# Kernel optimization log

Hardware: AMD Instinct MI355X
Metric: run time of the kernel (lower is better)

Reference implementation:

```python
import jax, jax.numpy as jnp
import numpy as np

B, L, C, D, H = 32, 4096, 64, 512, 720
EPS = 1e-5

def _xavier(key, shape):
    fan_in, fan_out = shape
    lim = float(np.sqrt(6.0 / (fan_in + fan_out)))
    return jax.random.uniform(key, shape, minval=-lim, maxval=lim, dtype=jnp.float32)

def setup_inputs() -> dict:
    key = jax.random.key(0)
    ks = jax.random.split(key, 8)
    return {
        "x": jax.random.normal(ks[0], (B, L, C), dtype=jnp.float32),
        "alpha": jnp.full((C,), 0.5, dtype=jnp.float32),
        "rev_w": jnp.ones((C,), dtype=jnp.float32),
        "rev_b": jnp.zeros((C,), dtype=jnp.float32),
        "se_w": _xavier(ks[1], (C, D)), "se_b": jnp.zeros((D,), jnp.float32),
        "sp_w": _xavier(ks[2], (D, C)), "sp_b": jnp.zeros((C,), jnp.float32),
        "st_w": _xavier(ks[3], (L, H)), "st_b": jnp.zeros((H,), jnp.float32),
        "te_w": _xavier(ks[4], (C, D)), "te_b": jnp.zeros((D,), jnp.float32),
        "tp_w": _xavier(ks[5], (D, C)), "tp_b": jnp.zeros((C,), jnp.float32),
        "tt_w": _xavier(ks[6], (L, H)), "tt_b": jnp.zeros((H,), jnp.float32),
    }

def _path(z, ew, eb, pw, pb, tw, tb):
    # z: (B,L,C) -> embed C->D -> (identity backbone) -> proj D->C -> temporal L->H
    h = z @ ew + eb            # (B,L,D)
    h = h @ pw + pb            # (B,L,C)
    h = jnp.einsum('blc,lh->bhc', h, tw) + tb[None, :, None]  # (B,H,C)
    return h

def reference(x, alpha, rev_w, rev_b, se_w, se_b, sp_w, sp_b, st_w, st_b,
              te_w, te_b, tp_w, tp_b, tt_w, tt_b):
    # RevIN norm (stats detached, var unbiased=False)
    mean = jax.lax.stop_gradient(jnp.mean(x, axis=1, keepdims=True))          # (B,1,C)
    stdev = jax.lax.stop_gradient(jnp.sqrt(jnp.var(x, axis=1, keepdims=True) + EPS))
    xn = (x - mean) / stdev * rev_w + rev_b
    # EMA decomposition: trend[t] = a*trend[t-1] + (1-a)*x[t], trend[0]=x[0]
    a = jax.nn.sigmoid(alpha)  # (C,)
    def step(carry, xt):
        nxt = a * carry + (1.0 - a) * xt
        return nxt, nxt
    t0 = xn[:, 0]                                    # (B,C)
    _, tr = jax.lax.scan(step, t0, jnp.swapaxes(xn, 0, 1)[1:])  # (L-1,B,C)
    trend = jnp.swapaxes(jnp.concatenate([t0[None], tr], axis=0), 0, 1)  # (B,L,C)
    seasonal = xn - trend
    out = _path(seasonal, se_w, se_b, sp_w, sp_b, st_w, st_b) \
        + _path(trend,    te_w, te_b, tp_w, tp_b, tt_w, tt_b)   # (B,H,C)
    # RevIN denorm
    out = (out - rev_b) / (rev_w + EPS)
    out = out * stdev + mean
    return out
```

## Files before the change

### kernel.cpp

```cpp
#include <hip/hip_runtime.h>
#include <hip/hip_bf16.h>
#include <string.h>
#include <stdint.h>

typedef __hip_bfloat16 bf16_t;
typedef float f32x4 __attribute__((ext_vector_type(4)));
typedef short bf16x8 __attribute__((ext_vector_type(8)));

static constexpr int Bn = 32, Ln = 4096, Cn = 64, Hn = 720, HPn = 768;
static constexpr float EPSf = 1e-5f;

static constexpr size_t OSR_SLICE = (size_t)Bn * Hn * Cn;

__device__ __forceinline__ short f2bf(float f) {
  bf16_t h = __float2bfloat16(f);
  unsigned short u; memcpy(&u, &h, 2);
  return (short)u;
}

__device__ __forceinline__ float sigm(float v) { return 1.f / (1.f + expf(-v)); }

__global__ void __launch_bounds__(256) k_pre(
    const float* __restrict__ se_w, const float* __restrict__ sp_w,
    const float* __restrict__ se_b, const float* __restrict__ sp_b,
    const float* __restrict__ te_w, const float* __restrict__ tp_w,
    const float* __restrict__ te_b, const float* __restrict__ tp_b,
    const float* __restrict__ st_w, const float* __restrict__ tt_w,
    const float* __restrict__ x, const float* __restrict__ alpha,
    float* __restrict__ M, float* __restrict__ cvec, bf16_t* __restrict__ Wt,
    float* __restrict__ Spart,
    float* __restrict__ Psub, float* __restrict__ Pseg,
    float* __restrict__ Ssum, float* __restrict__ Ssq) {
  __shared__ __align__(16) char smem[35072];
  int bid = blockIdx.x, t = threadIdx.x;

  if (bid < 2) {
    float (*ews)[68] = (float(*)[68])smem;
    float (*pws)[68] = (float(*)[68])(smem + 17408);
    float* ebs = (float*)(smem + 34816);
    int p = bid;
    const float* ew = p ? te_w : se_w;
    const float* pw = p ? tp_w : sp_w;
    const float* eb = p ? te_b : se_b;
    const float* pb = p ? tp_b : sp_b;
    int r0 = (t >> 4) * 4, c0 = (t & 15) * 4;
    float acc[4][4];
#pragma unroll
    for (int i = 0; i < 4; ++i)
#pragma unroll
      for (int j = 0; j < 4; ++j) acc[i][j] = 0.f;
    float cv = 0.f;
    for (int dc = 0; dc < 8; ++dc) {
      int d0 = dc * 64;
#pragma unroll
      for (int q = 0; q < 4; ++q) {
        int fi = t * 4 + q;
        int r = fi >> 4, dd = (fi * 4) & 63;
        *reinterpret_cast<f32x4*>(&ews[r][dd]) = *reinterpret_cast<const f32x4*>(&ew[r * 512 + d0 + dd]);
        *reinterpret_cast<f32x4*>(&pws[r][dd]) = *reinterpret_cast<const f32x4*>(&pw[(d0 + r) * 64 + dd]);
      }
      if (t < 64) ebs[t] = eb[d0 + t];
      __syncthreads();
#pragma unroll 4
      for (int g = 0; g < 16; ++g) {
        int dd = g * 4;
        f32x4 av[4], bv[4];
#pragma unroll
        for (int i = 0; i < 4; ++i) av[i] = *reinterpret_cast<const f32x4*>(&ews[r0 + i][dd]);
#pragma unroll
        for (int d = 0; d < 4; ++d) bv[d] = *reinterpret_cast<const f32x4*>(&pws[dd + d][c0]);
#pragma unroll
        for (int d = 0; d < 4; ++d)
#pragma unroll
          for (int i = 0; i < 4; ++i)
#pragma unroll
            for (int j = 0; j < 4; ++j) acc[i][j] = fmaf(av[i][d], bv[d][j], acc[i][j]);
      }
      if (t < 64) {
#pragma unroll 8
        for (int dd = 0; dd < 64; ++dd) cv = fmaf(ebs[dd], pws[dd][t], cv);
      }
      __syncthreads();
    }
#pragma unroll
    for (int i = 0; i < 4; ++i)
#pragma unroll
      for (int j = 0; j < 4; ++j)
        M[p * 4096 + (r0 + i) * 64 + c0 + j] = acc[i][j];
    if (t < 64) cvec[p * 64 + t] = cv + pb[t];

  } else if (bid < 514) {
    float (*lp)[64] = (float(*)[64])smem;
    float (*ls)[64] = (float(*)[64])(smem + 4096);
    float (*lq)[64] = (float(*)[64])(smem + 8192);
    int idx = bid - 2;
    int b = idx >> 4, sg = idx & 15;
    int ty = t >> 6, tx = t & 63;
    int s = sg * 4 + ty;
    int c4 = (tx & 15) * 4, sub = tx >> 4;
    float a[4], k1[4];
#pragma unroll
    for (int i = 0; i < 4; ++i) { a[i] = sigm(alpha[c4 + i]); k1[i] = 1.f - a[i]; }
    const float* xb = x + ((size_t)b * Ln + s * 64 + sub * 16) * Cn + c4;
    float pr[4] = {0.f, 0.f, 0.f, 0.f}, sm[4] = {0.f, 0.f, 0.f, 0.f}, sq[4] = {0.f, 0.f, 0.f, 0.f};
#pragma unroll
    for (int j = 0; j < 16; ++j) {
      f32x4 v = *reinterpret_cast<const f32x4*>(xb + (size_t)j * Cn);
#pragma unroll
      for (int i = 0; i < 4; ++i) {
        sm[i] += v[i];
        sq[i] = fmaf(v[i], v[i], sq[i]);
        pr[i] = fmaf(a[i], pr[i], k1[i] * v[i]);
      }
    }
    *reinterpret_cast<f32x4*>(&Psub[(((size_t)b * 64 + s) * 4 + sub) * 64 + c4]) =
        (f32x4){pr[0], pr[1], pr[2], pr[3]};
#pragma unroll
    for (int i = 0; i < 4; ++i) {
      lp[ty * 4 + sub][c4 + i] = pr[i];
      ls[ty * 4 + sub][c4 + i] = sm[i];
      lq[ty * 4 + sub][c4 + i] = sq[i];
    }
    __syncthreads();
    int c = tx;
    float av = sigm(alpha[c]);
    float a16 = av * av; a16 *= a16; a16 *= a16; a16 *= a16;
    float P = ((lp[ty * 4 + 0][c] * a16 + lp[ty * 4 + 1][c]) * a16 + lp[ty * 4 + 2][c]) * a16 + lp[ty * 4 + 3][c];
    int oidx = (b * 64 + s) * 64 + c;
    Pseg[oidx] = P;
    Ssum[oidx] = ls[ty * 4 + 0][c] + ls[ty * 4 + 1][c] + ls[ty * 4 + 2][c] + ls[ty * 4 + 3][c];
    Ssq[oidx]  = lq[ty * 4 + 0][c] + lq[ty * 4 + 1][c] + lq[ty * 4 + 2][c] + lq[ty * 4 + 3][c];

  } else {
    float (*tile)[65] = (float(*)[65])smem;
    float (*colsum)[64] = (float(*)[64])(smem + 16640);
    int idx = bid - 514;
    int p = idx / 768, rem = idx % 768;
    int lc = rem & 63, hc = rem >> 6;
    const float* W = p ? tt_w : st_w;
    int l0 = lc * 64, h0 = hc * 64;
    int row = t >> 6, col = t & 63;
    int h = h0 + col;
    float partial = 0.f;
    for (int r = row; r < 64; r += 4) {
      float v = (h < Hn) ? W[(size_t)(l0 + r) * Hn + h] : 0.f;
      tile[r][col] = v;
      partial += v;
    }
    colsum[row][col] = partial;
    __syncthreads();
    if (row == 0)
      Spart[((size_t)p * 64 + lc) * 768 + h] = colsum[0][col] + colsum[1][col] + colsum[2][col] + colsum[3][col];
    short* AF = (short*)Wt + (size_t)p * HPn * Ln;
#pragma unroll
    for (int u = 0; u < 2; ++u) {
      int uid = u * 256 + t;
      int ln = uid & 63, ktl = (uid >> 6) & 1, htl = uid >> 7;
      int fr = ln & 15, hi = ln >> 4;
      int ll = ktl * 32 + hi * 8;
      int hh = htl * 16 + fr;
      bf16x8 v;
#pragma unroll
      for (int e = 0; e < 8; ++e) v[e] = f2bf(tile[ll + e][hh]);
      size_t ht = (size_t)(h0 >> 4) + htl, ktg = (size_t)(l0 >> 5) + ktl;
      *reinterpret_cast<bf16x8*>(&AF[((ht * 128 + ktg) << 9) + ((size_t)ln << 3)]) = v;
    }
  }
}

__global__ void __launch_bounds__(256) k_mid(
    const float* __restrict__ x, const float* __restrict__ alpha,
    const float* __restrict__ rev_w, const float* __restrict__ rev_b,
    const float* __restrict__ Pseg, const float* __restrict__ Ssum, const float* __restrict__ Ssq,
    const float* __restrict__ Spart,
    float* __restrict__ mean, float* __restrict__ rstd, float* __restrict__ stdv,
    float* __restrict__ CarryIn, float* __restrict__ S) {
  int bid = blockIdx.x, t = threadIdx.x;
  if (bid < 8) {
    int b = bid * 4 + (t >> 6), c = t & 63;
    float sm = 0.f, sq = 0.f;
#pragma unroll 8
    for (int s = 0; s < 64; ++s) {
      int idx = (b * 64 + s) * 64 + c;
      sm += Ssum[idx]; sq += Ssq[idx];
    }
    float mn = sm * (1.f / 4096.f);
    float var = sq * (1.f / 4096.f) - mn * mn;
    float sd = sqrtf(var + EPSf);
    float rs = 1.f / sd;
    mean[b * 64 + c] = mn; stdv[b * 64 + c] = sd; rstd[b * 64 + c] = rs;

    float w = rev_w[c], rb = rev_b[c];
    float g = rs * w, d = rb - mn * g;
    float a = sigm(alpha[c]);
    float a2 = a * a, a4 = a2 * a2, a8 = a4 * a4, a16 = a8 * a8, a32 = a16 * a16;
    float a64 = a32 * a32;
    float dk1s = d * (1.f - a64);
    float carry = fmaf(g, x[((size_t)b * Ln) * Cn + c], d);
    for (int so = 0; so < 8; ++so) {
      float pv[8];
#pragma unroll
      for (int i = 0; i < 8; ++i)
        pv[i] = Pseg[((size_t)(b * 64 + so * 8 + i)) * 64 + c];
#pragma unroll
      for (int i = 0; i < 8; ++i) {
        CarryIn[((size_t)(b * 64 + so * 8 + i)) * 64 + c] = carry;
        carry = fmaf(a64, carry, fmaf(g, pv[i], dk1s));
      }
    }
  } else {
    int idx = (bid - 8) * 256 + t;
    int p = idx / 768, h = idx % 768;
    float s = 0.f;
#pragma unroll 8
    for (int lc = 0; lc < 64; ++lc)
      s += Spart[((size_t)p * 64 + lc) * 768 + h];
    S[p * 768 + h] = s;
  }
}

__global__ void __launch_bounds__(256) k_scanC(const float* __restrict__ x, const float* __restrict__ alpha,
                                               const float* __restrict__ rev_w, const float* __restrict__ rev_b,
                                               const float* __restrict__ mean, const float* __restrict__ rstd,
                                               const float* __restrict__ CarryIn, const float* __restrict__ Psub,
                                               bf16_t* __restrict__ Zt) {
  int b = blockIdx.x, ty = threadIdx.y, s = blockIdx.y * 4 + ty, t = threadIdx.x;
  int c4 = (t & 15) * 4, sub = t >> 4;
  float g[4], d[4], a[4], k1[4], a16[4], dk[4], tr[4];
#pragma unroll
  for (int i = 0; i < 4; ++i) {
    int c = c4 + i;
    float rs = rstd[b * 64 + c];
    g[i] = rs * rev_w[c]; d[i] = rev_b[c] - mean[b * 64 + c] * g[i];
    a[i] = sigm(alpha[c]); k1[i] = 1.f - a[i];
    float v = a[i] * a[i]; v *= v; v *= v; v *= v;
    a16[i] = v;
    dk[i] = d[i] * (1.f - v);
  }
  f32x4 cs = *reinterpret_cast<const f32x4*>(&CarryIn[((size_t)b * 64 + s) * 64 + c4]);
#pragma unroll
  for (int i = 0; i < 4; ++i) tr[i] = cs[i];
  for (int k = 0; k < sub; ++k) {
    f32x4 p = *reinterpret_cast<const f32x4*>(&Psub[(((size_t)b * 64 + s) * 4 + k) * 64 + c4]);
#pragma unroll
    for (int i = 0; i < 4; ++i) tr[i] = fmaf(a16[i], tr[i], fmaf(g[i], p[i], dk[i]));
  }
  const float* xb = x + ((size_t)b * Ln + s * 64 + sub * 16) * Cn + c4;
  bf16x8 vs[4][2], vt[4][2];
#pragma unroll
  for (int j = 0; j < 16; ++j) {
    f32x4 v = *reinterpret_cast<const f32x4*>(xb + (size_t)j * Cn);
#pragma unroll
    for (int i = 0; i < 4; ++i) {
      float xn = fmaf(g[i], v[i], d[i]);
      tr[i] = fmaf(a[i], tr[i], k1[i] * xn);
      vs[i][j >> 3][j & 7] = f2bf(xn - tr[i]);
      vt[i][j >> 3][j & 7] = f2bf(tr[i]);
    }
  }
  __shared__ short stage[4][8][520];
  short* BF0 = (short*)Zt;
  const size_t PATH = (size_t)Bn * Cn * Ln;
  int cq = (t & 15) >> 2;
  int u = cq * 2 + (sub >> 1);
  int hb = (sub & 1) * 2;
#pragma unroll
  for (int i = 0; i < 4; ++i) {
    int frv = (c4 & 15) + i;
    *reinterpret_cast<bf16x8*>(&stage[ty][u][(hb * 16 + frv) * 8]) = vs[i][0];
    *reinterpret_cast<bf16x8*>(&stage[ty][u][((hb + 1) * 16 + frv) * 8]) = vs[i][1];
  }
#pragma unroll
  for (int uu = 0; uu < 8; ++uu) {
    size_t nt = (size_t)b * 4 + (uu >> 1), ktg = (size_t)s * 2 + (uu & 1);
    *reinterpret_cast<bf16x8*>(BF0 + ((nt * 128 + ktg) << 9) + ((size_t)t << 3)) =
        *reinterpret_cast<const bf16x8*>(&stage[ty][uu][t * 8]);
  }
#pragma unroll
  for (int i = 0; i < 4; ++i) {
    int frv = (c4 & 15) + i;
    *reinterpret_cast<bf16x8*>(&stage[ty][u][(hb * 16 + frv) * 8]) = vt[i][0];
    *reinterpret_cast<bf16x8*>(&stage[ty][u][((hb + 1) * 16 + frv) * 8]) = vt[i][1];
  }
#pragma unroll
  for (int uu = 0; uu < 8; ++uu) {
    size_t nt = (size_t)b * 4 + (uu >> 1), ktg = (size_t)s * 2 + (uu & 1);
    *reinterpret_cast<bf16x8*>(BF0 + PATH + ((nt * 128 + ktg) << 9) + ((size_t)t << 3)) =
        *reinterpret_cast<const bf16x8*>(&stage[ty][uu][t * 8]);
  }
}

template <int KS>
__global__ void __launch_bounds__(256, 3) k_gemm(const bf16_t* __restrict__ Wt, const bf16_t* __restrict__ Zt,
                                                 float* __restrict__ Osr) {
  int per = gridDim.x >> 3;
  int swz = (blockIdx.x & 7) * per + (blockIdx.x >> 3);
  int z = swz / 96, rem = swz % 96;
  int by = rem >> 4, bx = rem & 15;
  int p = z / KS, kq = z % KS;
  const short* AF = (const short*)Wt + (size_t)p * HPn * Ln;
  const short* BF = (const short*)Zt + (size_t)p * (Bn * Cn) * Ln;
  int h0 = by * 128, n0 = bx * 128;
  int kbase = kq * (Ln / KS);
  const int NT = (Ln / KS) / 32;
  int tid = threadIdx.x, wid = tid >> 6, lane = tid & 63;
  int wr = wid >> 1, wc = wid & 1;
  int fr = lane & 15, hi = lane >> 4;
  const short* ab = AF + ((((size_t)(h0 >> 4) + wr * 4) * 128 + (kbase >> 5)) << 9) + ((size_t)lane << 3);
  const short* bb = BF + ((((size_t)(n0 >> 4) + wc * 4) * 128 + (kbase >> 5)) << 9) + ((size_t)lane << 3);

  f32x4 acc[4][4];
#pragma unroll
  for (int i = 0; i < 4; ++i)
#pragma unroll
    for (int j = 0; j < 4; ++j) acc[i][j] = (f32x4){0.f, 0.f, 0.f, 0.f};

  auto LOAD = [&](bf16x8 (&a)[4], bf16x8 (&b)[4], int kt) {
#pragma unroll
    for (int i = 0; i < 4; ++i)
      a[i] = *reinterpret_cast<const bf16x8*>(ab + (((size_t)i * 128 + kt) << 9));
#pragma unroll
    for (int j = 0; j < 4; ++j)
      b[j] = *reinterpret_cast<const bf16x8*>(bb + (((size_t)j * 128 + kt) << 9));
  };
  auto COMPUTE = [&](const bf16x8 (&a)[4], const bf16x8 (&b)[4]) {
    __builtin_amdgcn_s_setprio(1);
#pragma unroll
    for (int i = 0; i < 4; ++i)
#pragma unroll
      for (int j = 0; j < 4; ++j)
        acc[i][j] = __builtin_amdgcn_mfma_f32_16x16x32_bf16(a[i], b[j], acc[i][j], 0, 0, 0);
    __builtin_amdgcn_s_setprio(0);
  };

  bf16x8 aA[4], bA[4], aB[4], bB[4];
  LOAD(aA, bA, 0);
  for (int t = 0; t < NT; t += 2) {
    if (t + 1 < NT) LOAD(aB, bB, t + 1);
    __builtin_amdgcn_s_barrier();
    COMPUTE(aA, bA);
    if (t + 2 < NT) LOAD(aA, bA, t + 2);
    __builtin_amdgcn_s_barrier();
    if (t + 1 < NT) COMPUTE(aB, bB);
  }

#pragma unroll
  for (int i = 0; i < 4; ++i) {
#pragma unroll
    for (int j = 0; j < 4; ++j) {
#pragma unroll
      for (int r = 0; r < 4; ++r) {
        int m = wr * 64 + i * 16 + hi * 4 + r;
        int h = h0 + m;
        if (h < Hn) {
          int n = n0 + wc * 64 + j * 16 + fr;
          int bidx = n >> 6, c = n & 63;
          Osr[(((size_t)z * Bn + bidx) * Hn + h) * Cn + c] = acc[i][j][r];
        }
      }
    }
  }
}

template <int KS>
__global__ void __launch_bounds__(256) k_epi(const float* __restrict__ Osr, const float* __restrict__ M,
                                             const float* __restrict__ cvec, const float* __restrict__ S,
                                             const float* __restrict__ st_b, const float* __restrict__ tt_b,
                                             const float* __restrict__ rev_w, const float* __restrict__ rev_b,
                                             const float* __restrict__ mean, const float* __restrict__ stdv,
                                             float* __restrict__ out) {
  __shared__ float Msh[2][64][64];
  __shared__ float rowS[32][64];
  __shared__ float rowT[32][64];
  int t = threadIdx.x;
  for (int i = t; i < 2048; i += 256)
    reinterpret_cast<f32x4*>(Msh)[i] = reinterpret_cast<const f32x4*>(M)[i];
  int c = t & 63, grp = t >> 6;
  float w = rev_w[c], rb = rev_b[c];
  float cs = cvec[c], ct = cvec[64 + c];
  int base = blockIdx.x * 32;
#pragma unroll
  for (int k = 0; k < 8; ++k) {
    int rl = grp * 8 + k;
    int r = base + rl;
    int b = r / 720, h = r % 720;
    float vs = 0.f, vt = 0.f;
#pragma unroll
    for (int kq = 0; kq < KS; ++kq) {
      vs += Osr[(((size_t)kq * Bn + b) * Hn + h) * Cn + c];
      vt += Osr[(((size_t)(KS + kq) * Bn + b) * Hn + h) * Cn + c];
    }
    rowS[rl][c] = vs;
    rowT[rl][c] = vt;
  }
  __syncthreads();
  float acc[8];
  int hh[8], bb[8];
#pragma unroll
  for (int k = 0; k < 8; ++k) {
    int r = base + grp * 8 + k;
    bb[k] = r / 720; hh[k] = r % 720;
    acc[k] = cs * S[hh[k]] + ct * S[768 + hh[k]] + st_b[hh[k]] + tt_b[hh[k]];
  }
  int r0 = grp * 8;
  for (int cq = 0; cq < 16; ++cq) {
    f32x4 rs[8], rt[8];
#pragma unroll
    for (int k = 0; k < 8; ++k) rs[k] = *reinterpret_cast<const f32x4*>(&rowS[r0 + k][cq * 4]);
#pragma unroll
    for (int k = 0; k < 8; ++k) rt[k] = *reinterpret_cast<const f32x4*>(&rowT[r0 + k][cq * 4]);
#pragma unroll
    for (int i = 0; i < 4; ++i) {
      float m0 = Msh[0][cq * 4 + i][c], m1 = Msh[1][cq * 4 + i][c];
#pragma unroll
      for (int k = 0; k < 8; ++k)
        acc[k] = fmaf(rs[k][i], m0, fmaf(rt[k][i], m1, acc[k]));
    }
  }
  float winv = 1.f / (w + EPSf);
#pragma unroll
  for (int k = 0; k < 8; ++k) {
    float o = (acc[k] - rb) * winv * stdv[bb[k] * Cn + c] + mean[bb[k] * Cn + c];
    out[(size_t)(base + r0 + k) * 64 + c] = o;
  }
}

extern "C" void kernel_launch(void* const* d_in, const int* in_sizes, int n_in,
                              void* d_out, int out_size, void* d_ws, size_t ws_size,
                              hipStream_t stream) {
  const float* x     = (const float*)d_in[0];
  const float* alpha = (const float*)d_in[1];
  const float* rev_w = (const float*)d_in[2];
  const float* rev_b = (const float*)d_in[3];
  const float* se_w  = (const float*)d_in[4];
  const float* se_b  = (const float*)d_in[5];
  const float* sp_w  = (const float*)d_in[6];
  const float* sp_b  = (const float*)d_in[7];
  const float* st_w  = (const float*)d_in[8];
  const float* st_b  = (const float*)d_in[9];
  const float* te_w  = (const float*)d_in[10];
  const float* te_b  = (const float*)d_in[11];
  const float* tp_w  = (const float*)d_in[12];
  const float* tp_b  = (const float*)d_in[13];
  const float* tt_w  = (const float*)d_in[14];
  const float* tt_b  = (const float*)d_in[15];
  float* out = (float*)d_out;

  const size_t SZ_WT  = (size_t)2 * HPn * Ln * 2;
  const size_t SZ_ZT  = (size_t)2 * Bn * Cn * Ln * 2;
  const size_t SZ_SEG = (size_t)Bn * 64 * 64 * 4;
  const size_t SZ_M   = 2 * 64 * 64 * 4;
  const size_t SZ_CV  = 2 * 64 * 4;
  const size_t SZ_S   = 2 * 768 * 4;
  const size_t SZ_SP  = (size_t)2 * 64 * 768 * 4;
  const size_t TAIL   = SZ_M + SZ_CV + SZ_S + SZ_SP + 3 * (size_t)Bn * Cn * 4;

  const size_t NEED4 = SZ_WT + SZ_ZT + 8 * OSR_SLICE * 4 + TAIL;
  const int KS = (ws_size >= NEED4) ? 4 : 1;
  const size_t SZ_OSR = (size_t)(2 * KS) * OSR_SLICE * 4;

  char* ws = (char*)d_ws;
  bf16_t* Wt   = (bf16_t*)(ws);
  bf16_t* Zt   = (bf16_t*)(ws + SZ_WT);
  float*  Osr  = (float*)(ws + SZ_WT + SZ_ZT);
  float*  Psub  = Osr;
  float*  Pseg  = (float*)((char*)Psub + 4 * SZ_SEG);
  float*  Ssum  = (float*)((char*)Pseg + SZ_SEG);
  float*  Ssq   = (float*)((char*)Ssum + SZ_SEG);
  float*  Carry = (float*)((char*)Ssq + SZ_SEG);
  char* tail = ws + SZ_WT + SZ_ZT + SZ_OSR;
  float* Mbuf = (float*)tail;                 tail += SZ_M;
  float* cvec = (float*)tail;                 tail += SZ_CV;
  float* S    = (float*)tail;                 tail += SZ_S;
  float* Spart = (float*)tail;                tail += SZ_SP;
  float* mean = (float*)tail;                 tail += (size_t)Bn * Cn * 4;
  float* rstd = (float*)tail;                 tail += (size_t)Bn * Cn * 4;
  float* stdv = (float*)tail;

  k_pre<<<2050, 256, 0, stream>>>(se_w, sp_w, se_b, sp_b, te_w, tp_w, te_b, tp_b,
                                  st_w, tt_w, x, alpha, Mbuf, cvec, Wt, Spart,
                                  Psub, Pseg, Ssum, Ssq);
  k_mid<<<14, 256, 0, stream>>>(x, alpha, rev_w, rev_b, Pseg, Ssum, Ssq, Spart,
                                mean, rstd, stdv, Carry, S);
  k_scanC<<<dim3(32, 16), dim3(64, 4), 0, stream>>>(x, alpha, rev_w, rev_b, mean, rstd, Carry, Psub, Zt);
  if (KS == 4) {
    k_gemm<4><<<768, 256, 0, stream>>>(Wt, Zt, Osr);
    k_epi<4><<<720, 256, 0, stream>>>(Osr, Mbuf, cvec, S, st_b, tt_b, rev_w, rev_b, mean, stdv, out);
  } else {
    k_gemm<1><<<192, 256, 0, stream>>>(Wt, Zt, Osr);
    k_epi<1><<<720, 256, 0, stream>>>(Osr, Mbuf, cvec, S, st_b, tt_b, rev_w, rev_b, mean, stdv, out);
  }
}
```

Measured before the change: 108.0 us.

## Move weight-product and column-sum blocks off the critical path into GEMM launch

New measurement: 109.5 us. No clear change (+1.4%).

```diff
diff --git a/kernel.cpp b/kernel.cpp
--- a/kernel.cpp
+++ b/kernel.cpp
@@ -20,80 +20,67 @@
 
 __device__ __forceinline__ float sigm(float v) { return 1.f / (1.f + expf(-v)); }
 
-__global__ void __launch_bounds__(256) k_pre(
-    const float* __restrict__ se_w, const float* __restrict__ sp_w,
-    const float* __restrict__ se_b, const float* __restrict__ sp_b,
-    const float* __restrict__ te_w, const float* __restrict__ tp_w,
-    const float* __restrict__ te_b, const float* __restrict__ tp_b,
+__global__ void __launch_bounds__(256) k_preA(
     const float* __restrict__ st_w, const float* __restrict__ tt_w,
     const float* __restrict__ x, const float* __restrict__ alpha,
-    float* __restrict__ M, float* __restrict__ cvec, bf16_t* __restrict__ Wt,
-    float* __restrict__ Spart,
+    bf16_t* __restrict__ Wt, float* __restrict__ Spart,
     float* __restrict__ Psub, float* __restrict__ Pseg,
     float* __restrict__ Ssum, float* __restrict__ Ssq) {
-  __shared__ __align__(16) char smem[35072];
+  __shared__ __align__(16) char smem[20736];
   int bid = blockIdx.x, t = threadIdx.x;
 
-  if (bid < 2) {
-    float (*ews)[68] = (float(*)[68])smem;
-    float (*pws)[68] = (float(*)[68])(smem + 17408);
-    float* ebs = (float*)(smem + 34816);
-    int p = bid;
-    const float* ew = p ? te_w : se_w;
-    const float* pw = p ? tp_w : sp_w;
-    const float* eb = p ? te_b : se_b;
-    const float* pb = p ? tp_b : sp_b;
-    int r0 = (t >> 4) * 4, c0 = (t & 15) * 4;
-    float acc[4][4];
-#pragma unroll
-    for (int i = 0; i < 4; ++i)
-#pragma unroll
-      for (int j = 0; j < 4; ++j) acc[i][j] = 0.f;
-    float cv = 0.f;
-    for (int dc = 0; dc < 8; ++dc) {
-      int d0 = dc * 64;
-#pragma unroll
-      for (int q = 0; q < 4; ++q) {
-        int fi = t * 4 + q;
-        int r = fi >> 4, dd = (fi * 4) & 63;
-        *reinterpret_cast<f32x4*>(&ews[r][dd]) = *reinterpret_cast<const f32x4*>(&ew[r * 512 + d0 + dd]);
-        *reinterpret_cast<f32x4*>(&pws[r][dd]) = *reinterpret_cast<const f32x4*>(&pw[(d0 + r) * 64 + dd]);
+  if (bid < 1536) {
+    float (*tile)[65] = (float(*)[65])smem;
+    float (*cs16)[64] = (float(*)[64])(smem + 16640);
+    int p = bid / 768, rem = bid % 768;
+    int lc = rem & 63, hc = rem >> 6;
+    const float* W = p ? tt_w : st_w;
+    int l0 = lc * 64, h0 = hc * 64;
+    int g16 = t >> 4, c4l = (t & 15) * 4;
+    int h = h0 + c4l;
+    f32x4 ps = (f32x4){0.f, 0.f, 0.f, 0.f};
+#pragma unroll
+    for (int rr = 0; rr < 4; ++rr) {
+      int r = rr * 16 + g16;
+      const float* src = &W[(size_t)(l0 + r) * Hn + h];
+      f32x4 v;
+      if (h + 3 < Hn) {
+        v = *reinterpret_cast<const f32x4*>(src);
+      } else {
+#pragma unroll
+        for (int i = 0; i < 4; ++i) v[i] = (h + i < Hn) ? src[i] : 0.f;
       }
-      if (t < 64) ebs[t] = eb[d0 + t];
-      __syncthreads();
-#pragma unroll 4
-      for (int g = 0; g < 16; ++g) {
-        int dd = g * 4;
-        f32x4 av[4], bv[4];
-#pragma unroll
-        for (int i = 0; i < 4; ++i) av[i] = *reinterpret_cast<const f32x4*>(&ews[r0 + i][dd]);
-#pragma unroll
-        for (int d = 0; d < 4; ++d) bv[d] = *reinterpret_cast<const f32x4*>(&pws[dd + d][c0]);
-#pragma unroll
-        for (int d = 0; d < 4; ++d)
-#pragma unroll
-          for (int i = 0; i < 4; ++i)
-#pragma unroll
-            for (int j = 0; j < 4; ++j) acc[i][j] = fmaf(av[i][d], bv[d][j], acc[i][j]);
-      }
-      if (t < 64) {
-#pragma unroll 8
-        for (int dd = 0; dd < 64; ++dd) cv = fmaf(ebs[dd], pws[dd][t], cv);
-      }
-      __syncthreads();
-    }
-#pragma unroll
-    for (int i = 0; i < 4; ++i)
-#pragma unroll
-      for (int j = 0; j < 4; ++j)
-        M[p * 4096 + (r0 + i) * 64 + c0 + j] = acc[i][j];
-    if (t < 64) cvec[p * 64 + t] = cv + pb[t];
-
-  } else if (bid < 514) {
+      tile[r][c4l + 0] = v[0]; tile[r][c4l + 1] = v[1];
+      tile[r][c4l + 2] = v[2]; tile[r][c4l + 3] = v[3];
+      ps += v;
+    }
+    *reinterpret_cast<f32x4*>(&cs16[g16][c4l]) = ps;
+    __syncthreads();
+    if (t < 64) {
+      float s = 0.f;
+#pragma unroll
+      for (int g = 0; g < 16; ++g) s += cs16[g][t];
+      Spart[((size_t)p * 64 + lc) * 768 + h0 + t] = s;
+    }
+    short* AF = (short*)Wt + (size_t)p * HPn * Ln;
+#pragma unroll
+    for (int u = 0; u < 2; ++u) {
+      int uid = u * 256 + t;
+      int ln = uid & 63, ktl = (uid >> 6) & 1, htl = uid >> 7;
+      int fr = ln & 15, hi = ln >> 4;
+      int ll = ktl * 32 + hi * 8;
+      int hh = htl * 16 + fr;
+      bf16x8 v;
+#pragma unroll
+      for (int e = 0; e < 8; ++e) v[e] = f2bf(tile[ll + e][hh]);
+      size_t ht = (size_t)(h0 >> 4) + htl, ktg = (size_t)(l0 >> 5) + ktl;
+      *reinterpret_cast<bf16x8*>(&AF[((ht * 128 + ktg) << 9) + ((size_t)ln << 3)]) = v;
+    }
+  } else {
     float (*lp)[64] = (float(*)[64])smem;
     float (*ls)[64] = (float(*)[64])(smem + 4096);
     float (*lq)[64] = (float(*)[64])(smem + 8192);
-    int idx = bid - 2;
+    int idx = bid - 1536;
     int b = idx >> 4, sg = idx & 15;
     int ty = t >> 6, tx = t & 63;
     int s = sg * 4 + ty;
@@ -130,92 +117,45 @@
     Pseg[oidx] = P;
     Ssum[oidx] = ls[ty * 4 + 0][c] + ls[ty * 4 + 1][c] + ls[ty * 4 + 2][c] + ls[ty * 4 + 3][c];
     Ssq[oidx]  = lq[ty * 4 + 0][c] + lq[ty * 4 + 1][c] + lq[ty * 4 + 2][c] + lq[ty * 4 + 3][c];
-
-  } else {
-    float (*tile)[65] = (float(*)[65])smem;
-    float (*colsum)[64] = (float(*)[64])(smem + 16640);
-    int idx = bid - 514;
-    int p = idx / 768, rem = idx % 768;
-    int lc = rem & 63, hc = rem >> 6;
-    const float* W = p ? tt_w : st_w;
-    int l0 = lc * 64, h0 = hc * 64;
-    int row = t >> 6, col = t & 63;
-    int h = h0 + col;
-    float partial = 0.f;
-    for (int r = row; r < 64; r += 4) {
-      float v = (h < Hn) ? W[(size_t)(l0 + r) * Hn + h] : 0.f;
-      tile[r][col] = v;
-      partial += v;
-    }
-    colsum[row][col] = partial;
-    __syncthreads();
-    if (row == 0)
-      Spart[((size_t)p * 64 + lc) * 768 + h] = colsum[0][col] + colsum[1][col] + colsum[2][col] + colsum[3][col];
-    short* AF = (short*)Wt + (size_t)p * HPn * Ln;
-#pragma unroll
-    for (int u = 0; u < 2; ++u) {
-      int uid = u * 256 + t;
-      int ln = uid & 63, ktl = (uid >> 6) & 1, htl = uid >> 7;
-      int fr = ln & 15, hi = ln >> 4;
-      int ll = ktl * 32 + hi * 8;
-      int hh = htl * 16 + fr;
-      bf16x8 v;
-#pragma unroll
-      for (int e = 0; e < 8; ++e) v[e] = f2bf(tile[ll + e][hh]);
-      size_t ht = (size_t)(h0 >> 4) + htl, ktg = (size_t)(l0 >> 5) + ktl;
-      *reinterpret_cast<bf16x8*>(&AF[((ht * 128 + ktg) << 9) + ((size_t)ln << 3)]) = v;
-    }
-  }
-}
-
-__global__ void __launch_bounds__(256) k_mid(
+  }
+}
+
+__global__ void __launch_bounds__(256) k_scanB(
     const float* __restrict__ x, const float* __restrict__ alpha,
     const float* __restrict__ rev_w, const float* __restrict__ rev_b,
     const float* __restrict__ Pseg, const float* __restrict__ Ssum, const float* __restrict__ Ssq,
-    const float* __restrict__ Spart,
     float* __restrict__ mean, float* __restrict__ rstd, float* __restrict__ stdv,
-    float* __restrict__ CarryIn, float* __restrict__ S) {
-  int bid = blockIdx.x, t = threadIdx.x;
-  if (bid < 8) {
-    int b = bid * 4 + (t >> 6), c = t & 63;
-    float sm = 0.f, sq = 0.f;
+    float* __restrict__ CarryIn) {
+  int b = blockIdx.x * 4 + (threadIdx.x >> 6), c = threadIdx.x & 63;
+  float sm = 0.f, sq = 0.f;
 #pragma unroll 8
-    for (int s = 0; s < 64; ++s) {
-      int idx = (b * 64 + s) * 64 + c;
-      sm += Ssum[idx]; sq += Ssq[idx];
-    }
-    float mn = sm * (1.f / 4096.f);
-    float var = sq * (1.f / 4096.f) - mn * mn;
-    float sd = sqrtf(var + EPSf);
-    float rs = 1.f / sd;
-    mean[b * 64 + c] = mn; stdv[b * 64 + c] = sd; rstd[b * 64 + c] = rs;
-
-    float w = rev_w[c], rb = rev_b[c];
-    float g = rs * w, d = rb - mn * g;
-    float a = sigm(alpha[c]);
-    float a2 = a * a, a4 = a2 * a2, a8 = a4 * a4, a16 = a8 * a8, a32 = a16 * a16;
-    float a64 = a32 * a32;
-    float dk1s = d * (1.f - a64);
-    float carry = fmaf(g, x[((size_t)b * Ln) * Cn + c], d);
-    for (int so = 0; so < 8; ++so) {
-      float pv[8];
-#pragma unroll
-      for (int i = 0; i < 8; ++i)
-        pv[i] = Pseg[((size_t)(b * 64 + so * 8 + i)) * 64 + c];
-#pragma unroll
-      for (int i = 0; i < 8; ++i) {
-        CarryIn[((size_t)(b * 64 + so * 8 + i)) * 64 + c] = carry;
-        carry = fmaf(a64, carry, fmaf(g, pv[i], dk1s));
-      }
-    }
-  } else {
-    int idx = (bid - 8) * 256 + t;
-    int p = idx / 768, h = idx % 768;
-    float s = 0.f;
-#pragma unroll 8
-    for (int lc = 0; lc < 64; ++lc)
-      s += Spart[((size_t)p * 64 + lc) * 768 + h];
-    S[p * 768 + h] = s;
+  for (int s = 0; s < 64; ++s) {
+    int idx = (b * 64 + s) * 64 + c;
+    sm += Ssum[idx]; sq += Ssq[idx];
+  }
+  float mn = sm * (1.f / 4096.f);
+  float var = sq * (1.f / 4096.f) - mn * mn;
+  float sd = sqrtf(var + EPSf);
+  float rs = 1.f / sd;
+  mean[b * 64 + c] = mn; stdv[b * 64 + c] = sd; rstd[b * 64 + c] = rs;
+
+  float w = rev_w[c], rb = rev_b[c];
+  float g = rs * w, d = rb - mn * g;
+  float a = sigm(alpha[c]);
+  float a2 = a * a, a4 = a2 * a2, a8 = a4 * a4, a16 = a8 * a8, a32 = a16 * a16;
+  float a64 = a32 * a32;
+  float dk1s = d * (1.f - a64);
+  float carry = fmaf(g, x[((size_t)b * Ln) * Cn + c], d);
+  for (int so = 0; so < 8; ++so) {
+    float pv[8];
+#pragma unroll
+    for (int i = 0; i < 8; ++i)
+      pv[i] = Pseg[((size_t)(b * 64 + so * 8 + i)) * 64 + c];
+#pragma unroll
+    for (int i = 0; i < 8; ++i) {
+      CarryIn[((size_t)(b * 64 + so * 8 + i)) * 64 + c] = carry;
+      carry = fmaf(a64, carry, fmaf(g, pv[i], dk1s));
+    }
   }
 }
 
@@ -291,10 +231,88 @@
 }
 
 template <int KS>
-__global__ void __launch_bounds__(256, 3) k_gemm(const bf16_t* __restrict__ Wt, const bf16_t* __restrict__ Zt,
-                                                 float* __restrict__ Osr) {
-  int per = gridDim.x >> 3;
-  int swz = (blockIdx.x & 7) * per + (blockIdx.x >> 3);
+__global__ void __launch_bounds__(256, 3) k_gemm(
+    const bf16_t* __restrict__ Wt, const bf16_t* __restrict__ Zt, float* __restrict__ Osr,
+    const float* __restrict__ se_w, const float* __restrict__ sp_w,
+    const float* __restrict__ se_b, const float* __restrict__ sp_b,
+    const float* __restrict__ te_w, const float* __restrict__ tp_w,
+    const float* __restrict__ te_b, const float* __restrict__ tp_b,
+    const float* __restrict__ Spart,
+    float* __restrict__ M, float* __restrict__ cvec, float* __restrict__ S) {
+  constexpr int NG = (KS == 4) ? 768 : 192;
+  __shared__ __align__(16) char smem[35072];
+  int bid = blockIdx.x, t = threadIdx.x;
+
+  if (bid >= NG) {
+    int xb = bid - NG;
+    if (xb < 2) {
+      float (*ews)[68] = (float(*)[68])smem;
+      float (*pws)[68] = (float(*)[68])(smem + 17408);
+      float* ebs = (float*)(smem + 34816);
+      int p = xb;
+      const float* ew = p ? te_w : se_w;
+      const float* pw = p ? tp_w : sp_w;
+      const float* eb = p ? te_b : se_b;
+      const float* pb = p ? tp_b : sp_b;
+      int r0 = (t >> 4) * 4, c0 = (t & 15) * 4;
+      float acc[4][4];
+#pragma unroll
+      for (int i = 0; i < 4; ++i)
+#pragma unroll
+        for (int j = 0; j < 4; ++j) acc[i][j] = 0.f;
+      float cv = 0.f;
+      for (int dc = 0; dc < 8; ++dc) {
+        int d0 = dc * 64;
+#pragma unroll
+        for (int q = 0; q < 4; ++q) {
+          int fi = t * 4 + q;
+          int r = fi >> 4, dd = (fi * 4) & 63;
+          *reinterpret_cast<f32x4*>(&ews[r][dd]) = *reinterpret_cast<const f32x4*>(&ew[r * 512 + d0 + dd]);
+          *reinterpret_cast<f32x4*>(&pws[r][dd]) = *reinterpret_cast<const f32x4*>(&pw[(d0 + r) * 64 + dd]);
+        }
+        if (t < 64) ebs[t] = eb[d0 + t];
+        __syncthreads();
+#pragma unroll 4
+        for (int g = 0; g < 16; ++g) {
+          int dd = g * 4;
+          f32x4 av[4], bv[4];
+#pragma unroll
+          for (int i = 0; i < 4; ++i) av[i] = *reinterpret_cast<const f32x4*>(&ews[r0 + i][dd]);
+#pragma unroll
+          for (int d = 0; d < 4; ++d) bv[d] = *reinterpret_cast<const f32x4*>(&pws[dd + d][c0]);
+#pragma unroll
+          for (int d = 0; d < 4; ++d)
+#pragma unroll
+            for (int i = 0; i < 4; ++i)
+#pragma unroll
+              for (int j = 0; j < 4; ++j) acc[i][j] = fmaf(av[i][d], bv[d][j], acc[i][j]);
+        }
+        if (t < 64) {
+#pragma unroll 8
+          for (int dd = 0; dd < 64; ++dd) cv = fmaf(ebs[dd], pws[dd][t], cv);
+        }
+        __syncthreads();
+      }
+#pragma unroll
+      for (int i = 0; i < 4; ++i)
+#pragma unroll
+        for (int j = 0; j < 4; ++j)
+          M[p * 4096 + (r0 + i) * 64 + c0 + j] = acc[i][j];
+      if (t < 64) cvec[p * 64 + t] = cv + pb[t];
+    } else {
+      int idx = (xb - 2) * 256 + t;
+      int p = idx / 768, h = idx % 768;
+      float s = 0.f;
+#pragma unroll 8
+      for (int lc = 0; lc < 64; ++lc)
+        s += Spart[((size_t)p * 64 + lc) * 768 + h];
+      S[p * 768 + h] = s;
+    }
+    return;
+  }
+
+  constexpr int per = NG >> 3;
+  int swz = (bid & 7) * per + (bid >> 3);
   int z = swz / 96, rem = swz % 96;
   int by = rem >> 4, bx = rem & 15;
   int p = z / KS, kq = z % KS;
@@ -303,7 +321,7 @@
   int h0 = by * 128, n0 = bx * 128;
   int kbase = kq * (Ln / KS);
   const int NT = (Ln / KS) / 32;
-  int tid = threadIdx.x, wid = tid >> 6, lane = tid & 63;
+  int wid = t >> 6, lane = t & 63;
   int wr = wid >> 1, wc = wid & 1;
   int fr = lane & 15, hi = lane >> 4;
   const short* ab = AF + ((((size_t)(h0 >> 4) + wr * 4) * 128 + (kbase >> 5)) << 9) + ((size_t)lane << 3);
@@ -335,13 +353,13 @@
 
   bf16x8 aA[4], bA[4], aB[4], bB[4];
   LOAD(aA, bA, 0);
-  for (int t = 0; t < NT; t += 2) {
-    if (t + 1 < NT) LOAD(aB, bB, t + 1);
+  for (int tt = 0; tt < NT; tt += 2) {
+    if (tt + 1 < NT) LOAD(aB, bB, tt + 1);
     __builtin_amdgcn_s_barrier();
     COMPUTE(aA, bA);
-    if (t + 2 < NT) LOAD(aA, bA, t + 2);
+    if (tt + 2 < NT) LOAD(aA, bA, tt + 2);
     __builtin_amdgcn_s_barrier();
-    if (t + 1 < NT) COMPUTE(aB, bB);
+    if (tt + 1 < NT) COMPUTE(aB, bB);
   }
 
 #pragma unroll
@@ -477,17 +495,16 @@
   float* rstd = (float*)tail;                 tail += (size_t)Bn * Cn * 4;
   float* stdv = (float*)tail;
 
-  k_pre<<<2050, 256, 0, stream>>>(se_w, sp_w, se_b, sp_b, te_w, tp_w, te_b, tp_b,
-                                  st_w, tt_w, x, alpha, Mbuf, cvec, Wt, Spart,
-                                  Psub, Pseg, Ssum, Ssq);
-  k_mid<<<14, 256, 0, stream>>>(x, alpha, rev_w, rev_b, Pseg, Ssum, Ssq, Spart,
-                                mean, rstd, stdv, Carry, S);
+  k_preA<<<2048, 256, 0, stream>>>(st_w, tt_w, x, alpha, Wt, Spart, Psub, Pseg, Ssum, Ssq);
+  k_scanB<<<8, 256, 0, stream>>>(x, alpha, rev_w, rev_b, Pseg, Ssum, Ssq, mean, rstd, stdv, Carry);
   k_scanC<<<dim3(32, 16), dim3(64, 4), 0, stream>>>(x, alpha, rev_w, rev_b, mean, rstd, Carry, Psub, Zt);
   if (KS == 4) {
-    k_gemm<4><<<768, 256, 0, stream>>>(Wt, Zt, Osr);
+    k_gemm<4><<<776, 256, 0, stream>>>(Wt, Zt, Osr, se_w, sp_w, se_b, sp_b, te_w, tp_w, te_b, tp_b,
+                                       Spart, Mbuf, cvec, S);
     k_epi<4><<<720, 256, 0, stream>>>(Osr, Mbuf, cvec, S, st_b, tt_b, rev_w, rev_b, mean, stdv, out);
   } else {
-    k_gemm<1><<<192, 256, 0, stream>>>(Wt, Zt, Osr);
+    k_gemm<1><<<200, 256, 0, stream>>>(Wt, Zt, Osr, se_w, sp_w, se_b, sp_b, te_w, tp_w, te_b, tp_b,
+                                       Spart, Mbuf, cvec, S);
     k_epi<1><<<720, 256, 0, stream>>>(Osr, Mbuf, cvec, S, st_b, tt_b, rev_w, rev_b, mean, stdv, out);
   }
 }
```
